# Kernel tuning notes

Measured on AMD Instinct MI355X. Metric: run time of the kernel, lower is better.

## Reference

```python
import jax, jax.numpy as jnp
import numpy as np

B, K, D = 8192, 8192, 512


def setup_inputs() -> dict:
    key = jax.random.key(0)
    k1, k2 = jax.random.split(key)
    previous_residual = jax.random.normal(k1, (B, D), dtype=jnp.float32)
    codebook_embeddings = jax.random.normal(k2, (K, D), dtype=jnp.float32)
    return {"previous_residual": previous_residual,
            "codebook_embeddings": codebook_embeddings}


def reference(previous_residual, codebook_embeddings):
    # Squared Euclidean distances [B, K] via the expansion
    # subtract+square+sum, without materializing the [B, K, D] intermediate).
    x_sq = jnp.sum(previous_residual * previous_residual, axis=-1, keepdims=True)   # [B, 1]
    e_sq = jnp.sum(codebook_embeddings * codebook_embeddings, axis=-1)              # [K]
    cross = jnp.einsum('bd,kd->bk', previous_residual, codebook_embeddings)         # [B, K]
    distances = x_sq - 2.0 * cross + e_sq[None, :]                                  # [B, K]
    closest_codebook_index = jnp.argmin(distances, axis=1)                          # [B] int
    codebook_embedding = codebook_embeddings[closest_codebook_index]                # [B, D] gather
    next_residual = previous_residual - codebook_embedding                          # [B, D]
    return closest_codebook_index, next_residual
```

## Files before the change

### kernel.cpp

```cpp
#include <hip/hip_runtime.h>

#define Bn 8192
#define Kn 8192
#define Dn 512
#define WINDOW 0.25f

typedef _Float16 half8 __attribute__((ext_vector_type(8)));
typedef float floatx4 __attribute__((ext_vector_type(4)));
typedef unsigned long long u64;

__device__ __forceinline__ unsigned int fkey(float f) {
    unsigned int u = __float_as_uint(f);
    return (u & 0x80000000u) ? ~u : (u | 0x80000000u);
}

__device__ __forceinline__ void gld16(const _Float16* g, _Float16* l) {
    __builtin_amdgcn_global_load_lds(
        (const __attribute__((address_space(1))) unsigned int*)g,
        (__attribute__((address_space(3))) unsigned int*)l, 16, 0, 0);
}

__global__ __launch_bounds__(256) void esq_kernel(const float* __restrict__ E,
                                                  float* __restrict__ esq) {
    int wave = threadIdx.x >> 6;
    int lane = threadIdx.x & 63;
    int k = blockIdx.x * 4 + wave;
    const float4* row = (const float4*)(E + (size_t)k * Dn);
    float4 v0 = row[lane];
    float4 v1 = row[64 + lane];
    float s = v0.x*v0.x + v0.y*v0.y + v0.z*v0.z + v0.w*v0.w
            + v1.x*v1.x + v1.y*v1.y + v1.z*v1.z + v1.w*v1.w;
    #pragma unroll
    for (int off = 32; off > 0; off >>= 1) s += __shfl_down(s, off, 64);
    if (lane == 0) esq[k] = s;
}

__global__ __launch_bounds__(256) void convert_hi(
    const float* __restrict__ X, const float* __restrict__ E,
    _Float16* __restrict__ Xh, _Float16* __restrict__ Eh,
    float* __restrict__ esq)
{
    const bool isE = blockIdx.x >= 1024;
    const int pc = blockIdx.x & 1023;
    const int panel = pc >> 4;
    const int chunk = pc & 15;
    const float* src = isE ? E : X;
    _Float16* dst = isE ? Eh : Xh;
    const int t = threadIdx.x;
    const int row = t >> 1;
    const int kh  = (t & 1) * 16;
    const float* p = &src[(size_t)(panel * 128 + row) * Dn + chunk * 32 + kh];
    float4 v[4];
    v[0] = *(const float4*)(p + 0);
    v[1] = *(const float4*)(p + 4);
    v[2] = *(const float4*)(p + 8);
    v[3] = *(const float4*)(p + 12);
    const int slotbase = ((row >> 6) << 8) + (((row >> 4) & 3) << 6) + (row & 15);
    #pragma unroll
    for (int j = 0; j < 2; ++j) {
        half8 h;
        #pragma unroll
        for (int q = 0; q < 2; ++q) {
            const float4 w = v[j * 2 + q];
            h[q*4+0]=(_Float16)w.x; h[q*4+1]=(_Float16)w.y;
            h[q*4+2]=(_Float16)w.z; h[q*4+3]=(_Float16)w.w;
        }
        const int kq = (t & 1) * 2 + j;
        const size_t off = ((size_t)(panel * 16 + chunk) * 512
                            + slotbase + kq * 16) * 8;
        *(half8*)&dst[off] = h;
    }
    if (isE) {
        float s = 0.f;
        #pragma unroll
        for (int i = 0; i < 4; ++i)
            s += v[i].x*v[i].x + v[i].y*v[i].y + v[i].z*v[i].z + v[i].w*v[i].w;
        s += __shfl_xor(s, 1);
        if ((t & 1) == 0) atomicAdd(&esq[panel * 128 + row], s);
    }
}

__global__ __launch_bounds__(512, 4) void argmin_hi(
    const _Float16* __restrict__ Xh, const _Float16* __restrict__ Eh,
    const float* __restrict__ esq, float* __restrict__ bestf)
{
    __shared__ __align__(16) _Float16 sA[3][4096];

    const int tid  = threadIdx.x;
    const int bid  = blockIdx.x;
    const int bx   = bid & 31;
    const int by   = bid >> 5;
    const int lane = tid & 63, wave = tid >> 6;
    const int wm   = wave >> 2;
    const int wn   = wave & 3;
    const int colg = lane & 15, quad = lane >> 4;
    const int la8  = lane * 8;

    const _Float16* gA = Xh + (size_t)by * 65536 + tid * 8;
    const _Float16* gB = Eh + (size_t)(2 * bx + (wn >> 1)) * 65536
                            + (wn & 1) * 2048 + la8;

    auto stageA = [&](int t, int b) {
        gld16(gA + t * 4096, &sA[b][tid * 8]);
    };

    floatx4 acc[4][4];
    #pragma unroll
    for (int i = 0; i < 4; ++i)
        #pragma unroll
        for (int j = 0; j < 4; ++j) acc[i][j] = {0.f, 0.f, 0.f, 0.f};

    stageA(0, 0);
    stageA(1, 1);

    #pragma unroll
    for (int t = 0; t < 16; ++t) {
        const int b = t % 3;
        if (t < 15) asm volatile("s_waitcnt vmcnt(1)" ::: "memory");
        else        asm volatile("s_waitcnt vmcnt(0)" ::: "memory");
        __builtin_amdgcn_s_barrier();

        half8 bb[4];
        #pragma unroll
        for (int ni = 0; ni < 4; ++ni)
            bb[ni] = *(const half8*)(gB + t * 4096 + ni * 512);
        if (t + 2 < 16) stageA(t + 2, (t + 2) % 3);

        const _Float16* A0 = &sA[b][wm * 2048 + la8];
        half8 a[4];
        #pragma unroll
        for (int mi = 0; mi < 4; ++mi) a[mi] = *(const half8*)&A0[mi * 512];

        __builtin_amdgcn_s_setprio(1);
        #pragma unroll
        for (int mi = 0; mi < 4; ++mi)
            #pragma unroll
            for (int ni = 0; ni < 4; ++ni)
                acc[mi][ni] = __builtin_amdgcn_mfma_f32_16x16x32_f16(
                    a[mi], bb[ni], acc[mi][ni], 0, 0, 0);
        __builtin_amdgcn_s_setprio(0);
    }

    float2* sm = (float2*)&sA[1][0];
    const int n0 = bx * 256 + wn * 64;
    float eqv[4];
    #pragma unroll
    for (int ni = 0; ni < 4; ++ni) eqv[ni] = esq[n0 + ni * 16 + colg];
    const unsigned ob_base = ((unsigned)colg << 4) | ((unsigned)wn << 2);

    #pragma unroll
    for (int mi = 0; mi < 4; ++mi)
        #pragma unroll
        for (int r = 0; r < 4; ++r) {
            float w1 = INFINITY, w2 = INFINITY;
            #pragma unroll
            for (int ni = 0; ni < 4; ++ni) {
                const float dv = eqv[ni] - 2.0f * acc[mi][ni][r];
                const float key = __uint_as_float(
                    (__float_as_uint(dv) & 0xFFFFFF00u) | (ob_base | (unsigned)ni));
                w2 = fminf(w2, fmaxf(w1, key));
                w1 = fminf(w1, key);
            }
            #pragma unroll
            for (int off = 1; off < 16; off <<= 1) {
                const float p1 = __shfl_xor(w1, off);
                const float p2 = __shfl_xor(w2, off);
                w2 = fminf(fmaxf(w1, p1), fminf(w2, p2));
                w1 = fminf(w1, p1);
            }
            if (colg == 0) {
                const int row128 = wm * 64 + mi * 16 + quad * 4 + r;
                float2 st; st.x = w1; st.y = w2;
                sm[row128 * 4 + wn] = st;
            }
        }
    __syncthreads();
    if (tid < 128) {
        float m1 = INFINITY, m2 = INFINITY;
        #pragma unroll
        for (int w = 0; w < 4; ++w) {
            const float2 p = sm[tid * 4 + w];
            m2 = fminf(fmaxf(m1, p.x), fminf(m2, p.y));
            m1 = fminf(m1, p.x);
        }
        float2 st; st.x = m1; st.y = m2;
        *(float2*)&bestf[(size_t)(by * 128 + tid) * 64 + bx * 2] = st;
    }
}

__global__ __launch_bounds__(256) void refine_kernel(
    const float* __restrict__ X, const float* __restrict__ E,
    const float* __restrict__ bestf, float* __restrict__ out)
{
    const int lane = threadIdx.x & 63, wave = threadIdx.x >> 6;
    const int b = blockIdx.x * 4 + wave;

    const float val = bestf[(size_t)b * 64 + lane];
    const unsigned bits = __float_as_uint(val);
    const int cb = lane >> 1;
    const int colg = (bits >> 4) & 15, wn = (bits >> 2) & 3, ni = bits & 3;
    const int col = cb * 256 + wn * 64 + ni * 16 + colg;

    float mn = val;
    #pragma unroll
    for (int off = 1; off < 64; off <<= 1) mn = fminf(mn, __shfl_xor(mn, off));

    const float4* xr = (const float4*)(X + (size_t)b * Dn);
    const float4 x0 = xr[lane * 2], x1 = xr[lane * 2 + 1];

    u64 bestk = ~0ull;
    float4 be0, be1;
    u64 mask = __ballot(val <= mn + WINDOW);
    while (mask) {
        const int s = __builtin_ctzll(mask);
        mask &= mask - 1;
        const int c = __shfl(col, s);
        const float4* er = (const float4*)(E + (size_t)c * Dn);
        const float4 e0 = er[lane * 2], e1 = er[lane * 2 + 1];
        float p = e0.x*(e0.x - 2.f*x0.x) + e0.y*(e0.y - 2.f*x0.y)
                + e0.z*(e0.z - 2.f*x0.z) + e0.w*(e0.w - 2.f*x0.w)
                + e1.x*(e1.x - 2.f*x1.x) + e1.y*(e1.y - 2.f*x1.y)
                + e1.z*(e1.z - 2.f*x1.z) + e1.w*(e1.w - 2.f*x1.w);
        #pragma unroll
        for (int off = 1; off < 64; off <<= 1) p += __shfl_xor(p, off);
        const u64 k = ((u64)fkey(p) << 32) | (u64)(unsigned int)c;
        if (k < bestk) { bestk = k; be0 = e0; be1 = e1; }
    }

    const int idx = (int)(unsigned int)(bestk & 0xFFFFFFFFull);
    if (lane == 0) out[b] = (float)idx;
    float4 r0, r1;
    r0.x = x0.x - be0.x; r0.y = x0.y - be0.y; r0.z = x0.z - be0.z; r0.w = x0.w - be0.w;
    r1.x = x1.x - be1.x; r1.y = x1.y - be1.y; r1.z = x1.z - be1.z; r1.w = x1.w - be1.w;
    float4* o = (float4*)(out + Bn + (size_t)b * Dn);
    o[lane * 2] = r0; o[lane * 2 + 1] = r1;
}

#define KSPLIT 16
#define LDSW 132
__global__ __launch_bounds__(256, 2) void argmin_fp32(
    const float* __restrict__ X, const float* __restrict__ E,
    const float* __restrict__ esq, u64* __restrict__ best)
{
    __shared__ __align__(16) float Xs[16][LDSW];
    __shared__ __align__(16) float Es[16][LDSW];
    __shared__ u64 red[128][16];
    const int tid = threadIdx.x;
    const int tx = tid & 15, ty = tid >> 4;
    const int rowTile = blockIdx.x / KSPLIT;
    const int split   = blockIdx.x % KSPLIT;
    const int m0 = rowTile * 128;
    const int kbase = split * (Kn / KSPLIT);
    float bestv[8]; int besti[8];
    #pragma unroll
    for (int i = 0; i < 8; ++i) { bestv[i] = INFINITY; besti[i] = 0; }
    const int ldRow = tid >> 2, ldD = (tid & 3) * 4;
    for (int kt = 0; kt < (Kn / KSPLIT) / 128; ++kt) {
        const int k0 = kbase + kt * 128;
        float acc[8][8] = {};
        for (int dc = 0; dc < Dn / 16; ++dc) {
            const int d0 = dc * 16;
            float4 xa = *(const float4*)&X[(size_t)(m0 + ldRow)      * Dn + d0 + ldD];
            float4 xb = *(const float4*)&X[(size_t)(m0 + 64 + ldRow) * Dn + d0 + ldD];
            float4 ea = *(const float4*)&E[(size_t)(k0 + ldRow)      * Dn + d0 + ldD];
            float4 eb = *(const float4*)&E[(size_t)(k0 + 64 + ldRow) * Dn + d0 + ldD];
            __syncthreads();
            Xs[ldD+0][ldRow] = xa.x; Xs[ldD+1][ldRow] = xa.y;
            Xs[ldD+2][ldRow] = xa.z; Xs[ldD+3][ldRow] = xa.w;
            Xs[ldD+0][64+ldRow] = xb.x; Xs[ldD+1][64+ldRow] = xb.y;
            Xs[ldD+2][64+ldRow] = xb.z; Xs[ldD+3][64+ldRow] = xb.w;
            Es[ldD+0][ldRow] = ea.x; Es[ldD+1][ldRow] = ea.y;
            Es[ldD+2][ldRow] = ea.z; Es[ldD+3][ldRow] = ea.w;
            Es[ldD+0][64+ldRow] = eb.x; Es[ldD+1][64+ldRow] = eb.y;
            Es[ldD+2][64+ldRow] = eb.z; Es[ldD+3][64+ldRow] = eb.w;
            __syncthreads();
            #pragma unroll
            for (int d = 0; d < 16; ++d) {
                float a8[8], b8[8];
                *(float4*)&a8[0] = *(const float4*)&Xs[d][4*ty];
                *(float4*)&a8[4] = *(const float4*)&Xs[d][64 + 4*ty];
                *(float4*)&b8[0] = *(const float4*)&Es[d][4*tx];
                *(float4*)&b8[4] = *(const float4*)&Es[d][64 + 4*tx];
                #pragma unroll
                for (int i = 0; i < 8; ++i)
                    #pragma unroll
                    for (int j = 0; j < 8; ++j) acc[i][j] += a8[i] * b8[j];
            }
        }
        #pragma unroll
        for (int j = 0; j < 8; ++j) {
            const int c = k0 + ((j < 4) ? (4*tx + j) : (64 + 4*tx + (j - 4)));
            const float eq = esq[c];
            #pragma unroll
            for (int i = 0; i < 8; ++i) {
                float dval = eq - 2.0f * acc[i][j];
                if (dval < bestv[i]) { bestv[i] = dval; besti[i] = c; }
            }
        }
    }
    #pragma unroll
    for (int i = 0; i < 8; ++i) {
        int rloc = (i < 4) ? (4*ty + i) : (64 + 4*ty + (i - 4));
        red[rloc][tx] = ((u64)fkey(bestv[i]) << 32) | (u64)(unsigned int)besti[i];
    }
    __syncthreads();
    if (tid < 128) {
        u64 m = red[tid][0];
        #pragma unroll
        for (int t = 1; t < 16; ++t) { u64 v = red[tid][t]; if (v < m) m = v; }
        best[(size_t)(m0 + tid) * KSPLIT + split] = m;
    }
}

__global__ __launch_bounds__(256) void finalize_kernel(
    const float* __restrict__ X, const float* __restrict__ E,
    const u64* __restrict__ best, float* __restrict__ out, int nsplits)
{
    __shared__ int sidx[2];
    const int half = threadIdx.x >> 7;
    const int t    = threadIdx.x & 127;
    const int b    = blockIdx.x * 2 + half;
    if (t < 64) {
        u64 v = (t < nsplits) ? best[(size_t)b * nsplits + t] : ~0ull;
        #pragma unroll
        for (int off = 1; off < 64; off <<= 1) {
            u64 o = __shfl_xor(v, off);
            if (o < v) v = o;
        }
        if (t == 0) {
            int idx = (int)(unsigned int)(v & 0xFFFFFFFFull);
            sidx[half] = idx;
            out[b] = (float)idx;
        }
    }
    __syncthreads();
    const int idx = sidx[half];
    float4 x = ((const float4*)(X + (size_t)b * Dn))[t];
    float4 e = ((const float4*)(E + (size_t)idx * Dn))[t];
    float4 r; r.x = x.x - e.x; r.y = x.y - e.y; r.z = x.z - e.z; r.w = x.w - e.w;
    ((float4*)(out + Bn + (size_t)b * Dn))[t] = r;
}

extern "C" void kernel_launch(void* const* d_in, const int* in_sizes, int n_in,
                              void* d_out, int out_size, void* d_ws, size_t ws_size,
                              hipStream_t stream) {
    const float* X = (const float*)d_in[0];
    const float* E = (const float*)d_in[1];
    float* out = (float*)d_out;

    const size_t HB = (size_t)Bn * Dn * sizeof(_Float16);
    const size_t BESTB = (size_t)Bn * 64 * sizeof(float);
    const size_t NEED = 32768 + 2 * HB + BESTB;

    float* esq = (float*)d_ws;

    if (ws_size >= NEED) {
        _Float16* Xh = (_Float16*)((char*)d_ws + 32768);
        _Float16* Eh = (_Float16*)((char*)d_ws + 32768 + HB);
        float* bestf = (float*)((char*)d_ws + 32768 + 2 * HB);
        hipMemsetAsync((void*)esq, 0, Kn * sizeof(float), stream);
        convert_hi<<<2048, 256, 0, stream>>>(X, E, Xh, Eh, esq);
        argmin_hi<<<2048, 512, 0, stream>>>(Xh, Eh, esq, bestf);
        refine_kernel<<<Bn / 4, 256, 0, stream>>>(X, E, bestf, out);
    } else {
        u64* best = (u64*)((char*)d_ws + 32768);
        esq_kernel<<<Kn / 4, 256, 0, stream>>>(E, esq);
        argmin_fp32<<<(Bn / 128) * KSPLIT, 256, 0, stream>>>(X, E, esq, best);
        finalize_kernel<<<Bn / 2, 256, 0, stream>>>(X, E, best, out, KSPLIT);
    }
}
```

Measured before the change: 168.8 us.

## Deepen the X-tile LDS pipeline to six stages with two k-chunks per barrier

The argmin GEMM main loop now uses six LDS buffers for the X tiles, prefetching four chunks ahead instead of two. Each iteration handles two k-chunks under one barrier and one vmcnt wait, with both sets of codebook fragments loaded up front. The aim is to halve the number of barriers and hide more global-load latency. The cost is double the shared memory per block (about 48 KB), which may cut the number of resident blocks per CU below the launch-bounds target. It also raises register pressure from the extra fragment registers.

```diff
diff --git a/kernel.cpp b/kernel.cpp
--- a/kernel.cpp
+++ b/kernel.cpp
@@ -84,7 +84,7 @@
     const _Float16* __restrict__ Xh, const _Float16* __restrict__ Eh,
     const float* __restrict__ esq, float* __restrict__ bestf)
 {
-    __shared__ __align__(16) _Float16 sA[3][4096];
+    __shared__ __align__(16) _Float16 sA[6][4096];
 
     const int tid  = threadIdx.x;
     const int bid  = blockIdx.x;
@@ -100,8 +100,8 @@
     const _Float16* gB = Eh + (size_t)(2 * bx + (wn >> 1)) * 65536
                             + (wn & 1) * 2048 + la8;
 
-    auto stageA = [&](int t, int b) {
-        gld16(gA + t * 4096, &sA[b][tid * 8]);
+    auto stageA = [&](int t, int s) {
+        gld16(gA + t * 4096, &sA[s][tid * 8]);
     };
 
     floatx4 acc[4][4];
@@ -110,38 +110,52 @@
         #pragma unroll
         for (int j = 0; j < 4; ++j) acc[i][j] = {0.f, 0.f, 0.f, 0.f};
 
-    stageA(0, 0);
-    stageA(1, 1);
-
-    #pragma unroll
-    for (int t = 0; t < 16; ++t) {
-        const int b = t % 3;
-        if (t < 15) asm volatile("s_waitcnt vmcnt(1)" ::: "memory");
-        else        asm volatile("s_waitcnt vmcnt(0)" ::: "memory");
+    stageA(0, 0); stageA(1, 1); stageA(2, 2); stageA(3, 3);
+
+    #pragma unroll
+    for (int i = 0; i < 8; ++i) {
+        const int c0 = 2 * i, c1 = 2 * i + 1;
+        const int s0 = c0 % 6, s1 = c1 % 6;
+        asm volatile("s_waitcnt vmcnt(2)" ::: "memory");
         __builtin_amdgcn_s_barrier();
 
-        half8 bb[4];
+        half8 bb0[4], bb1[4];
         #pragma unroll
         for (int ni = 0; ni < 4; ++ni)
-            bb[ni] = *(const half8*)(gB + t * 4096 + ni * 512);
-        if (t + 2 < 16) stageA(t + 2, (t + 2) % 3);
-
-        const _Float16* A0 = &sA[b][wm * 2048 + la8];
+            bb0[ni] = *(const half8*)(gB + c0 * 4096 + ni * 512);
+        #pragma unroll
+        for (int ni = 0; ni < 4; ++ni)
+            bb1[ni] = *(const half8*)(gB + c1 * 4096 + ni * 512);
+        if (c0 + 4 < 16) stageA(c0 + 4, (c0 + 4) % 6);
+        if (c1 + 4 < 16) stageA(c1 + 4, (c1 + 4) % 6);
+
+        const _Float16* A0 = &sA[s0][wm * 2048 + la8];
         half8 a[4];
         #pragma unroll
         for (int mi = 0; mi < 4; ++mi) a[mi] = *(const half8*)&A0[mi * 512];
-
         __builtin_amdgcn_s_setprio(1);
         #pragma unroll
         for (int mi = 0; mi < 4; ++mi)
             #pragma unroll
             for (int ni = 0; ni < 4; ++ni)
                 acc[mi][ni] = __builtin_amdgcn_mfma_f32_16x16x32_f16(
-                    a[mi], bb[ni], acc[mi][ni], 0, 0, 0);
+                    a[mi], bb0[ni], acc[mi][ni], 0, 0, 0);
         __builtin_amdgcn_s_setprio(0);
-    }
-
-    float2* sm = (float2*)&sA[1][0];
+
+        const _Float16* A1 = &sA[s1][wm * 2048 + la8];
+        #pragma unroll
+        for (int mi = 0; mi < 4; ++mi) a[mi] = *(const half8*)&A1[mi * 512];
+        __builtin_amdgcn_s_setprio(1);
+        #pragma unroll
+        for (int mi = 0; mi < 4; ++mi)
+            #pragma unroll
+            for (int ni = 0; ni < 4; ++ni)
+                acc[mi][ni] = __builtin_amdgcn_mfma_f32_16x16x32_f16(
+                    a[mi], bb1[ni], acc[mi][ni], 0, 0, 0);
+        __builtin_amdgcn_s_setprio(0);
+    }
+
+    float2* sm = (float2*)&sA[0][0];
     const int n0 = bx * 256 + wn * 64;
     float eqv[4];
     #pragma unroll
```

Result: no change. 167.8 us (-0.6%).
